# Kernel tuning notes

Measured on AMD Instinct MI355X. Metric: run time of the kernel, lower is better.

## Reference

```python
import jax, jax.numpy as jnp
import numpy as np

N = 50000
E = 800000
D = 256
C = 8
H = 64
LN_EPS = 1e-5


def setup_inputs() -> dict:
    key = jax.random.key(0)
    ks = jax.random.split(key, 8)
    x = jax.random.normal(ks[0], (N, D), dtype=jnp.float32)
    edge_index = jax.random.randint(ks[1], (2, E), 0, N, dtype=jnp.int64)
    omega = jax.random.uniform(ks[2], (E, C), dtype=jnp.float32)
    # xavier-uniform-ish parameter init
    def xavier(k, shape, fan_in, fan_out):
        a = float(np.sqrt(6.0 / (fan_in + fan_out)))
        return jax.random.uniform(k, shape, dtype=jnp.float32, minval=-a, maxval=a)
    proj = xavier(ks[3], (D, C, H), D, C * H)          # layer-0 projection
    W1 = xavier(ks[4], (C, H, H), H, H)                # layer-0 channel weights
    W2 = xavier(ks[5], (C, H, H), H, H)                # layer-1 channel weights
    ln_gamma = jnp.ones((H,), dtype=jnp.float32)
    ln_beta = jnp.zeros((H,), dtype=jnp.float32)
    return {"x": x, "edge_index": edge_index, "omega": omega,
            "proj": proj, "W1": W1, "W2": W2,
            "ln_gamma": ln_gamma, "ln_beta": ln_beta}


def _conv(h, src, dst, omega, W):
    # h: [N, C, H]; per-channel weighted scatter-add then channel-specific bmm.
    outs = []
    for c in range(C):  # small fixed channel loop, mirrors original structure
        msg = omega[:, c, None] * h[src, c, :]                  # [E, H]
        outs.append(jax.ops.segment_sum(msg, dst, num_segments=N))
    h_next = jnp.stack(outs, axis=1)                            # [N, C, H]
    return jnp.einsum('nch,cho->nco', h_next, W)                # channel bmm


def _layernorm(h, gamma, beta):
    mu = jnp.mean(h, axis=-1, keepdims=True)
    var = jnp.mean(jnp.square(h - mu), axis=-1, keepdims=True)
    return (h - mu) * jax.lax.rsqrt(var + LN_EPS) * gamma + beta


def reference(x, edge_index, omega, proj, W1, W2, ln_gamma, ln_beta):
    src, dst = edge_index[0], edge_index[1]
    # layer 0: project raw features into channel space [N, C, H]
    h = (x @ proj.reshape(D, C * H)).reshape(N, C, H)
    h = _conv(h, src, dst, omega, W1)
    h = _layernorm(h, ln_gamma, ln_beta)
    h = jax.nn.relu(h)
    # layer 1 (last layer: no ReLU)
    h = _conv(h, src, dst, omega, W2)
    h = _layernorm(h, ln_gamma, ln_beta)
    return h
```

## Files before the change

kernel.cpp:

```cpp
#include <hip/hip_runtime.h>

#define NN 50000
#define NE 800000
#define DD 256
#define CC 8
#define HH 64
#define CHW 512
#define LN_EPS 1e-5f
#define SCAN_BLOCKS ((NN + 1023) / 1024)

typedef __attribute__((ext_vector_type(8))) __bf16 bf16x8;
typedef __attribute__((ext_vector_type(4))) float f32x4;

__device__ inline ushort f2bf(float f) {
  uint u = __float_as_uint(f);
  return (ushort)((u + 0x7fffu + ((u >> 16) & 1u)) >> 16);
}

__device__ inline float omw_decode(uint w, int hi) {
  ushort hu = hi ? (ushort)(w >> 16) : (ushort)(w & 0xffffu);
  union { ushort u; _Float16 f; } cv; cv.u = hu;
  return (float)cv.f;
}

__device__ inline void acc8(float* acc, uint4 hv, float wt) {
  acc[0] += wt * __uint_as_float(hv.x << 16);
  acc[1] += wt * __uint_as_float(hv.x & 0xffff0000u);
  acc[2] += wt * __uint_as_float(hv.y << 16);
  acc[3] += wt * __uint_as_float(hv.y & 0xffff0000u);
  acc[4] += wt * __uint_as_float(hv.z << 16);
  acc[5] += wt * __uint_as_float(hv.z & 0xffff0000u);
  acc[6] += wt * __uint_as_float(hv.w << 16);
  acc[7] += wt * __uint_as_float(hv.w & 0xffff0000u);
}

__global__ __launch_bounds__(256) void fold_w1_kernel(
    const float* __restrict__ proj, const float* __restrict__ W1,
    ushort* __restrict__ projW1T) {
  __shared__ float wl[64];
  const int n = blockIdx.x;
  const int c = n >> 6, i = n & 63;
  const int tid = threadIdx.x;
  if (tid < 64) wl[tid] = W1[c * 4096 + tid * 64 + i];
  __syncthreads();
  const float* pr = proj + (size_t)tid * 512 + c * 64;
  float acc = 0.f;
#pragma unroll
  for (int k = 0; k < 64; ++k) acc += pr[k] * wl[k];
  projW1T[(size_t)n * 256 + tid] = f2bf(acc);
}

__global__ __launch_bounds__(256) void w2t_kernel(const float* __restrict__ W2,
                                                  ushort* __restrict__ W2T) {
  int c = blockIdx.x;
  for (int idx = threadIdx.x; idx < 4096; idx += 256) {
    int nn = idx >> 6, k = idx & 63;
    W2T[(size_t)c * 4096 + idx] = f2bf(W2[(size_t)c * 4096 + k * 64 + nn]);
  }
}

__global__ __launch_bounds__(256) void gemm_proj_kernel(
    const float* __restrict__ x, const ushort* __restrict__ BT,
    ushort* __restrict__ gout) {
  __shared__ ushort As[128 * 40];
  __shared__ ushort Bs[128 * 40];
  const int tid = threadIdx.x;
  const int lane = tid & 63, wv = tid >> 6;
  const int wm = wv >> 1, wn = wv & 1;
  const int lr = lane & 15, kg = lane >> 4;
  const int row0 = blockIdx.x * 128;
  const int col0 = blockIdx.y * 128;

  f32x4 acc[4][4];
#pragma unroll
  for (int i = 0; i < 4; ++i)
#pragma unroll
    for (int j = 0; j < 4; ++j) acc[i][j] = (f32x4){0.f, 0.f, 0.f, 0.f};

  for (int kk = 0; kk < 8; ++kk) {
    __syncthreads();
#pragma unroll
    for (int i = 0; i < 4; ++i) {
      int idx = tid + i * 256;
      int row = idx >> 3, quad = idx & 7;
      int rg = row0 + row;
      rg = rg < NN ? rg : NN - 1;
      float4 v = *(const float4*)(x + (size_t)rg * 256 + kk * 32 + quad * 4);
      ushort4 o = {f2bf(v.x), f2bf(v.y), f2bf(v.z), f2bf(v.w)};
      *(ushort4*)(As + row * 40 + quad * 4) = o;
    }
#pragma unroll
    for (int i = 0; i < 2; ++i) {
      int idx = tid + i * 256;
      int n = idx >> 2, quad = idx & 3;
      uint4 v = *(const uint4*)(BT + (size_t)(col0 + n) * 256 + kk * 32 + quad * 8);
      *(uint4*)(Bs + n * 40 + quad * 8) = v;
    }
    __syncthreads();
    bf16x8 a[4], b[4];
#pragma unroll
    for (int i = 0; i < 4; ++i)
      a[i] = *(const bf16x8*)(As + (wm * 64 + i * 16 + lr) * 40 + kg * 8);
#pragma unroll
    for (int j = 0; j < 4; ++j)
      b[j] = *(const bf16x8*)(Bs + (wn * 64 + j * 16 + lr) * 40 + kg * 8);
#pragma unroll
    for (int i = 0; i < 4; ++i)
#pragma unroll
      for (int j = 0; j < 4; ++j)
        acc[i][j] = __builtin_amdgcn_mfma_f32_16x16x32_bf16(a[i], b[j], acc[i][j], 0, 0, 0);
  }

  const int orow = kg * 4;
  const int ocol = lane & 15;
#pragma unroll
  for (int i = 0; i < 4; ++i) {
    int rg0 = row0 + wm * 64 + i * 16 + orow;
#pragma unroll
    for (int q = 0; q < 4; ++q) {
      int rg = rg0 + q;
      if (rg < NN) {
#pragma unroll
        for (int j = 0; j < 4; ++j) {
          gout[(size_t)rg * 512 + col0 + wn * 64 + j * 16 + ocol] = f2bf(acc[i][j][q]);
        }
      }
    }
  }
}

__global__ __launch_bounds__(256) void bmm_g_kernel(
    const ushort* __restrict__ h, const ushort* __restrict__ WT,
    ushort* __restrict__ g) {
  __shared__ ushort As[128 * 72];
  __shared__ ushort Bs[64 * 72];
  __shared__ float Cs[4][32 * 68];
  const int tid = threadIdx.x, lane = tid & 63, wv = tid >> 6;
  const int lr = lane & 15, kg = lane >> 4;
  const int n0 = blockIdx.x * 128;
  const int c = blockIdx.y;

#pragma unroll
  for (int i = 0; i < 4; ++i) {
    int idx = tid + i * 256;
    int row = idx >> 3, q = idx & 7;
    int rg = n0 + row;
    rg = rg < NN ? rg : NN - 1;
    *(uint4*)(As + row * 72 + q * 8) =
        *(const uint4*)(h + (size_t)rg * 512 + c * 64 + q * 8);
  }
#pragma unroll
  for (int i = 0; i < 2; ++i) {
    int idx = tid + i * 256;
    int row = idx >> 3, q = idx & 7;
    *(uint4*)(Bs + row * 72 + q * 8) =
        *(const uint4*)(WT + (size_t)c * 4096 + row * 64 + q * 8);
  }
  __syncthreads();

  f32x4 acc[2][4];
#pragma unroll
  for (int m = 0; m < 2; ++m)
#pragma unroll
    for (int j = 0; j < 4; ++j) acc[m][j] = (f32x4){0.f, 0.f, 0.f, 0.f};

#pragma unroll
  for (int ks = 0; ks < 2; ++ks) {
    bf16x8 a[2], b[4];
#pragma unroll
    for (int m = 0; m < 2; ++m)
      a[m] = *(const bf16x8*)(As + (wv * 32 + m * 16 + lr) * 72 + ks * 32 + kg * 8);
#pragma unroll
    for (int j = 0; j < 4; ++j)
      b[j] = *(const bf16x8*)(Bs + (j * 16 + lr) * 72 + ks * 32 + kg * 8);
#pragma unroll
    for (int m = 0; m < 2; ++m)
#pragma unroll
      for (int j = 0; j < 4; ++j)
        acc[m][j] = __builtin_amdgcn_mfma_f32_16x16x32_bf16(a[m], b[j], acc[m][j], 0, 0, 0);
  }

  float* cs = &Cs[wv][0];
#pragma unroll
  for (int m = 0; m < 2; ++m)
#pragma unroll
    for (int j = 0; j < 4; ++j)
#pragma unroll
      for (int q = 0; q < 4; ++q)
        cs[(m * 16 + kg * 4 + q) * 68 + j * 16 + lr] = acc[m][j][q];
  __syncthreads();

  const int row = lane & 31, half = lane >> 5;
  const int rg = n0 + wv * 32 + row;
  if (rg < NN) {
    const float* rp = cs + row * 68 + half * 32;
    ushort ob[32];
#pragma unroll
    for (int t = 0; t < 32; ++t) ob[t] = f2bf(rp[t]);
    ushort* op = g + (size_t)rg * 512 + c * 64 + half * 32;
#pragma unroll
    for (int t = 0; t < 4; ++t)
      *(uint4*)(op + t * 8) = *(uint4*)(ob + t * 8);
  }
}

__global__ void hist_kernel(const int* __restrict__ dst, int* __restrict__ cnt) {
  int e = blockIdx.x * 256 + threadIdx.x;
  if (e < NE) atomicAdd(&cnt[dst[e]], 1);
}

__global__ __launch_bounds__(1024) void scan1_kernel(const int* __restrict__ cnt,
                                                     int* __restrict__ blocksum) {
  __shared__ int ws[16];
  int tid = threadIdx.x, t = blockIdx.x * 1024 + tid;
  int v = (t < NN) ? cnt[t] : 0;
#pragma unroll
  for (int off = 32; off; off >>= 1) v += __shfl_xor(v, off);
  if ((tid & 63) == 0) ws[tid >> 6] = v;
  __syncthreads();
  if (tid < 16) {
    int s = ws[tid];
#pragma unroll
    for (int off = 8; off; off >>= 1) s += __shfl_xor(s, off, 16);
    if (tid == 0) blocksum[blockIdx.x] = s;
  }
}

__global__ __launch_bounds__(64) void scan2_kernel(int* __restrict__ blocksum,
                                                   int* __restrict__ rowptr) {
  int tid = threadIdx.x;
  int v = (tid < SCAN_BLOCKS) ? blocksum[tid] : 0;
  int orig = v;
#pragma unroll
  for (int off = 1; off < 64; off <<= 1) {
    int u = __shfl_up(v, off);
    if (tid >= off) v += u;
  }
  if (tid < SCAN_BLOCKS) blocksum[tid] = v - orig;
  if (tid == 63) rowptr[NN] = v;
}

__global__ __launch_bounds__(1024) void scan3_kernel(const int* __restrict__ blocksum,
                                                     int* __restrict__ cntcur,
                                                     int* __restrict__ rowptr) {
  __shared__ int ws[16];
  int tid = threadIdx.x, lane = tid & 63, wv = tid >> 6;
  int t = blockIdx.x * 1024 + tid;
  int orig = (t < NN) ? cntcur[t] : 0;
  int v = orig;
#pragma unroll
  for (int off = 1; off < 64; off <<= 1) {
    int u = __shfl_up(v, off);
    if (lane >= off) v += u;
  }
  if (lane == 63) ws[wv] = v;
  __syncthreads();
  if (tid < 16) {
    int s = ws[tid];
#pragma unroll
    for (int off = 1; off < 16; off <<= 1) {
      int u = __shfl_up(s, off, 16);
      if (tid >= off) s += u;
    }
    ws[tid] = s;
  }
  __syncthreads();
  if (t < NN) {
    int excl = blocksum[blockIdx.x] + (wv ? ws[wv - 1] : 0) + (v - orig);
    rowptr[t] = excl;
    cntcur[t] = excl;
  }
}

__global__ void fill_kernel(const int* __restrict__ dst, const int* __restrict__ src,
                            const float* __restrict__ omega, int* __restrict__ cursor,
                            int* __restrict__ esrc, uint4* __restrict__ eom) {
  int e = blockIdx.x * 256 + threadIdx.x;
  if (e < NE) {
    int d = dst[e];
    int pos = atomicAdd(&cursor[d], 1);
    esrc[pos] = src[e];
    const float4* om4 = (const float4*)(omega + (size_t)e * 8);
    float4 o0 = om4[0], o1 = om4[1];
    union { _Float16 f[8]; uint4 v; } pk;
    pk.f[0] = (_Float16)o0.x; pk.f[1] = (_Float16)o0.y;
    pk.f[2] = (_Float16)o0.z; pk.f[3] = (_Float16)o0.w;
    pk.f[4] = (_Float16)o1.x; pk.f[5] = (_Float16)o1.y;
    pk.f[6] = (_Float16)o1.z; pk.f[7] = (_Float16)o1.w;
    eom[pos] = pk.v;
  }
}

template <bool RELU, bool BF16OUT>
__global__ __launch_bounds__(256) void conv_ln_kernel(
    const ushort* __restrict__ g, const int* __restrict__ esrc,
    const uint* __restrict__ eomw, const int* __restrict__ rowptr,
    const float* __restrict__ gamma, const float* __restrict__ beta,
    void* __restrict__ outv) {
  int n = blockIdx.x * 4 + (threadIdx.x >> 6);
  if (n >= NN) return;
  const int lane = threadIdx.x & 63;
  const int c = lane >> 3;
  const int hi = c & 1;
  const int cw = c >> 1;
  const int i0 = (lane & 7) * 8;
  int start = rowptr[n], end = rowptr[n + 1];
  const uint4* g4 = (const uint4*)g;
  float acc[8] = {0.f, 0.f, 0.f, 0.f, 0.f, 0.f, 0.f, 0.f};

  int idx = start;
  for (; idx + 7 < end; idx += 8) {
    int s0 = esrc[idx + 0], s1 = esrc[idx + 1], s2 = esrc[idx + 2], s3 = esrc[idx + 3];
    int s4 = esrc[idx + 4], s5 = esrc[idx + 5], s6 = esrc[idx + 6], s7 = esrc[idx + 7];
    uint4 h0 = g4[(size_t)s0 * 64 + lane];
    uint4 h1 = g4[(size_t)s1 * 64 + lane];
    uint4 h2 = g4[(size_t)s2 * 64 + lane];
    uint4 h3 = g4[(size_t)s3 * 64 + lane];
    uint4 h4 = g4[(size_t)s4 * 64 + lane];
    uint4 h5 = g4[(size_t)s5 * 64 + lane];
    uint4 h6 = g4[(size_t)s6 * 64 + lane];
    uint4 h7 = g4[(size_t)s7 * 64 + lane];
    float w0 = omw_decode(eomw[(idx + 0) * 4 + cw], hi);
    float w1 = omw_decode(eomw[(idx + 1) * 4 + cw], hi);
    float w2 = omw_decode(eomw[(idx + 2) * 4 + cw], hi);
    float w3 = omw_decode(eomw[(idx + 3) * 4 + cw], hi);
    float w4 = omw_decode(eomw[(idx + 4) * 4 + cw], hi);
    float w5 = omw_decode(eomw[(idx + 5) * 4 + cw], hi);
    float w6 = omw_decode(eomw[(idx + 6) * 4 + cw], hi);
    float w7 = omw_decode(eomw[(idx + 7) * 4 + cw], hi);
    acc8(acc, h0, w0); acc8(acc, h1, w1); acc8(acc, h2, w2); acc8(acc, h3, w3);
    acc8(acc, h4, w4); acc8(acc, h5, w5); acc8(acc, h6, w6); acc8(acc, h7, w7);
  }
  for (; idx + 3 < end; idx += 4) {
    int s0 = esrc[idx + 0], s1 = esrc[idx + 1], s2 = esrc[idx + 2], s3 = esrc[idx + 3];
    uint4 h0 = g4[(size_t)s0 * 64 + lane];
    uint4 h1 = g4[(size_t)s1 * 64 + lane];
    uint4 h2 = g4[(size_t)s2 * 64 + lane];
    uint4 h3 = g4[(size_t)s3 * 64 + lane];
    float w0 = omw_decode(eomw[(idx + 0) * 4 + cw], hi);
    float w1 = omw_decode(eomw[(idx + 1) * 4 + cw], hi);
    float w2 = omw_decode(eomw[(idx + 2) * 4 + cw], hi);
    float w3 = omw_decode(eomw[(idx + 3) * 4 + cw], hi);
    acc8(acc, h0, w0); acc8(acc, h1, w1); acc8(acc, h2, w2); acc8(acc, h3, w3);
  }
  for (; idx < end; ++idx) {
    int s = esrc[idx];
    uint4 hv = g4[(size_t)s * 64 + lane];
    acc8(acc, hv, omw_decode(eomw[idx * 4 + cw], hi));
  }

  float s8 = ((acc[0] + acc[1]) + (acc[2] + acc[3])) +
             ((acc[4] + acc[5]) + (acc[6] + acc[7]));
  s8 += __shfl_xor(s8, 1);
  s8 += __shfl_xor(s8, 2);
  s8 += __shfl_xor(s8, 4);
  float mu = s8 * (1.f / 64.f);
  float d[8];
  float v = 0.f;
#pragma unroll
  for (int j = 0; j < 8; ++j) {
    d[j] = acc[j] - mu;
    v += d[j] * d[j];
  }
  v += __shfl_xor(v, 1);
  v += __shfl_xor(v, 2);
  v += __shfl_xor(v, 4);
  float inv = rsqrtf(v * (1.f / 64.f) + LN_EPS);
  float4 g0 = *(const float4*)(gamma + i0);
  float4 g1 = *(const float4*)(gamma + i0 + 4);
  float4 b0 = *(const float4*)(beta + i0);
  float4 b1 = *(const float4*)(beta + i0 + 4);
  float gg[8] = {g0.x, g0.y, g0.z, g0.w, g1.x, g1.y, g1.z, g1.w};
  float bb[8] = {b0.x, b0.y, b0.z, b0.w, b1.x, b1.y, b1.z, b1.w};
  float y[8];
#pragma unroll
  for (int j = 0; j < 8; ++j) {
    float t = d[j] * inv * gg[j] + bb[j];
    y[j] = RELU ? fmaxf(t, 0.f) : t;
  }
  if (BF16OUT) {
    ushort o[8];
#pragma unroll
    for (int j = 0; j < 8; ++j) o[j] = f2bf(y[j]);
    *(uint4*)((ushort*)outv + (size_t)n * 512 + c * 64 + i0) = *(uint4*)o;
  } else {
    float* op = (float*)outv + (size_t)n * 512 + c * 64 + i0;
    *(float4*)op = make_float4(y[0], y[1], y[2], y[3]);
    *(float4*)(op + 4) = make_float4(y[4], y[5], y[6], y[7]);
  }
}

extern "C" void kernel_launch(void* const* d_in, const int* in_sizes, int n_in,
                              void* d_out, int out_size, void* d_ws, size_t ws_size,
                              hipStream_t stream) {
  const float* x     = (const float*)d_in[0];
  const int*   edge  = (const int*)d_in[1];
  const float* omega = (const float*)d_in[2];
  const float* proj  = (const float*)d_in[3];
  const float* W1    = (const float*)d_in[4];
  const float* W2    = (const float*)d_in[5];
  const float* gamma = (const float*)d_in[6];
  const float* beta  = (const float*)d_in[7];
  const int* src = edge;
  const int* dst = edge + NE;

  char* p = (char*)d_ws;
  ushort* hbf    = (ushort*)p;              p += (size_t)NN * CHW * 2;
  uint4*  eom    = (uint4*)p;               p += (size_t)NE * 16;
  int*    esrc   = (int*)p;                 p += (size_t)NE * 4;
  int*    rowptr = (int*)p;                 p += (size_t)(NN + 16) * 4;
  int*    cntcur = (int*)p;                 p += (size_t)(NN + 16) * 4;
  int*    blocksum=(int*)p;                 p += (size_t)64 * 4;
  ushort* projW1T= (ushort*)p;              p += (size_t)512 * 256 * 2;
  ushort* W2T    = (ushort*)p;

  ushort* h1 = (ushort*)d_out;

  hipMemsetAsync(cntcur, 0, NN * sizeof(int), stream);
  hist_kernel<<<(NE + 255) / 256, 256, 0, stream>>>(dst, cntcur);
  scan1_kernel<<<SCAN_BLOCKS, 1024, 0, stream>>>(cntcur, blocksum);
  scan2_kernel<<<1, 64, 0, stream>>>(blocksum, rowptr);
  scan3_kernel<<<SCAN_BLOCKS, 1024, 0, stream>>>(blocksum, cntcur, rowptr);
  fill_kernel<<<(NE + 255) / 256, 256, 0, stream>>>(dst, src, omega, cntcur, esrc, eom);

  fold_w1_kernel<<<512, 256, 0, stream>>>(proj, W1, projW1T);
  w2t_kernel<<<8, 256, 0, stream>>>(W2, W2T);

  gemm_proj_kernel<<<dim3((NN + 127) / 128, 4), 256, 0, stream>>>(x, projW1T, hbf);
  conv_ln_kernel<true, true><<<(NN + 3) / 4, 256, 0, stream>>>(
      hbf, esrc, (const uint*)eom, rowptr, gamma, beta, h1);

  bmm_g_kernel<<<dim3((NN + 127) / 128, CC), 256, 0, stream>>>(h1, W2T, hbf);
  conv_ln_kernel<false, false><<<(NN + 3) / 4, 256, 0, stream>>>(
      hbf, esrc, (const uint*)eom, rowptr, gamma, beta, d_out);
}
```

Measured before the change: 414.3 us.

## Switch intermediates to channel-major layout and split conv per channel

Intermediate bf16 features are stored channel-major ([C][N][64]) instead of node-major, and the conv+layernorm kernel now launches one block per (4-node group, channel) with each lane handling one feature element. Consecutive blocks that share a channel gather from a 6.4 MB slice instead of the full 51 MB tensor, aiming for better L2 locality on the random gathers. In exchange, each edge's src index and omega weight are now read eight times across blocks, each lane loads 2 bytes instead of 16, and the block count grows eightfold.

After: 605.0 us. +46.0%, slower.

```diff
diff --git a/kernel.cpp b/kernel.cpp
--- a/kernel.cpp
+++ b/kernel.cpp
@@ -17,21 +17,14 @@
   return (ushort)((u + 0x7fffu + ((u >> 16) & 1u)) >> 16);
 }
 
+__device__ inline float b2f(ushort v) {
+  return __uint_as_float(((uint)v) << 16);
+}
+
 __device__ inline float omw_decode(uint w, int hi) {
   ushort hu = hi ? (ushort)(w >> 16) : (ushort)(w & 0xffffu);
   union { ushort u; _Float16 f; } cv; cv.u = hu;
   return (float)cv.f;
-}
-
-__device__ inline void acc8(float* acc, uint4 hv, float wt) {
-  acc[0] += wt * __uint_as_float(hv.x << 16);
-  acc[1] += wt * __uint_as_float(hv.x & 0xffff0000u);
-  acc[2] += wt * __uint_as_float(hv.y << 16);
-  acc[3] += wt * __uint_as_float(hv.y & 0xffff0000u);
-  acc[4] += wt * __uint_as_float(hv.z << 16);
-  acc[5] += wt * __uint_as_float(hv.z & 0xffff0000u);
-  acc[6] += wt * __uint_as_float(hv.w << 16);
-  acc[7] += wt * __uint_as_float(hv.w & 0xffff0000u);
 }
 
 __global__ __launch_bounds__(256) void fold_w1_kernel(
@@ -122,7 +115,9 @@
       if (rg < NN) {
 #pragma unroll
         for (int j = 0; j < 4; ++j) {
-          gout[(size_t)rg * 512 + col0 + wn * 64 + j * 16 + ocol] = f2bf(acc[i][j][q]);
+          int cc = col0 + wn * 64 + j * 16 + ocol;
+          int ch = cc >> 6, ii = cc & 63;
+          gout[((size_t)ch * NN + rg) * 64 + ii] = f2bf(acc[i][j][q]);
         }
       }
     }
@@ -139,6 +134,8 @@
   const int lr = lane & 15, kg = lane >> 4;
   const int n0 = blockIdx.x * 128;
   const int c = blockIdx.y;
+  const ushort* hc = h + (size_t)c * NN * 64;
+  ushort* gc = g + (size_t)c * NN * 64;
 
 #pragma unroll
   for (int i = 0; i < 4; ++i) {
@@ -146,8 +143,7 @@
     int row = idx >> 3, q = idx & 7;
     int rg = n0 + row;
     rg = rg < NN ? rg : NN - 1;
-    *(uint4*)(As + row * 72 + q * 8) =
-        *(const uint4*)(h + (size_t)rg * 512 + c * 64 + q * 8);
+    *(uint4*)(As + row * 72 + q * 8) = *(const uint4*)(hc + (size_t)rg * 64 + q * 8);
   }
 #pragma unroll
   for (int i = 0; i < 2; ++i) {
@@ -197,7 +193,7 @@
     ushort ob[32];
 #pragma unroll
     for (int t = 0; t < 32; ++t) ob[t] = f2bf(rp[t]);
-    ushort* op = g + (size_t)rg * 512 + c * 64 + half * 32;
+    ushort* op = gc + (size_t)rg * 64 + half * 32;
 #pragma unroll
     for (int t = 0; t < 4; ++t)
       *(uint4*)(op + t * 8) = *(uint4*)(ob + t * 8);
@@ -297,29 +293,29 @@
     const uint* __restrict__ eomw, const int* __restrict__ rowptr,
     const float* __restrict__ gamma, const float* __restrict__ beta,
     void* __restrict__ outv) {
-  int n = blockIdx.x * 4 + (threadIdx.x >> 6);
+  const int bid = blockIdx.x;
+  const int c = bid & 7;
+  const int n = (bid >> 3) * 4 + (threadIdx.x >> 6);
   if (n >= NN) return;
   const int lane = threadIdx.x & 63;
-  const int c = lane >> 3;
   const int hi = c & 1;
   const int cw = c >> 1;
-  const int i0 = (lane & 7) * 8;
   int start = rowptr[n], end = rowptr[n + 1];
-  const uint4* g4 = (const uint4*)g;
-  float acc[8] = {0.f, 0.f, 0.f, 0.f, 0.f, 0.f, 0.f, 0.f};
+  const ushort* gc = g + (size_t)c * NN * 64;
+  float acc = 0.f;
 
   int idx = start;
   for (; idx + 7 < end; idx += 8) {
     int s0 = esrc[idx + 0], s1 = esrc[idx + 1], s2 = esrc[idx + 2], s3 = esrc[idx + 3];
     int s4 = esrc[idx + 4], s5 = esrc[idx + 5], s6 = esrc[idx + 6], s7 = esrc[idx + 7];
-    uint4 h0 = g4[(size_t)s0 * 64 + lane];
-    uint4 h1 = g4[(size_t)s1 * 64 + lane];
-    uint4 h2 = g4[(size_t)s2 * 64 + lane];
-    uint4 h3 = g4[(size_t)s3 * 64 + lane];
-    uint4 h4 = g4[(size_t)s4 * 64 + lane];
-    uint4 h5 = g4[(size_t)s5 * 64 + lane];
-    uint4 h6 = g4[(size_t)s6 * 64 + lane];
-    uint4 h7 = g4[(size_t)s7 * 64 + lane];
+    ushort v0 = gc[(size_t)s0 * 64 + lane];
+    ushort v1 = gc[(size_t)s1 * 64 + lane];
+    ushort v2 = gc[(size_t)s2 * 64 + lane];
+    ushort v3 = gc[(size_t)s3 * 64 + lane];
+    ushort v4 = gc[(size_t)s4 * 64 + lane];
+    ushort v5 = gc[(size_t)s5 * 64 + lane];
+    ushort v6 = gc[(size_t)s6 * 64 + lane];
+    ushort v7 = gc[(size_t)s7 * 64 + lane];
     float w0 = omw_decode(eomw[(idx + 0) * 4 + cw], hi);
     float w1 = omw_decode(eomw[(idx + 1) * 4 + cw], hi);
     float w2 = omw_decode(eomw[(idx + 2) * 4 + cw], hi);
@@ -328,65 +324,44 @@
     float w5 = omw_decode(eomw[(idx + 5) * 4 + cw], hi);
     float w6 = omw_decode(eomw[(idx + 6) * 4 + cw], hi);
     float w7 = omw_decode(eomw[(idx + 7) * 4 + cw], hi);
-    acc8(acc, h0, w0); acc8(acc, h1, w1); acc8(acc, h2, w2); acc8(acc, h3, w3);
-    acc8(acc, h4, w4); acc8(acc, h5, w5); acc8(acc, h6, w6); acc8(acc, h7, w7);
+    acc += w0 * b2f(v0); acc += w1 * b2f(v1);
+    acc += w2 * b2f(v2); acc += w3 * b2f(v3);
+    acc += w4 * b2f(v4); acc += w5 * b2f(v5);
+    acc += w6 * b2f(v6); acc += w7 * b2f(v7);
   }
   for (; idx + 3 < end; idx += 4) {
     int s0 = esrc[idx + 0], s1 = esrc[idx + 1], s2 = esrc[idx + 2], s3 = esrc[idx + 3];
-    uint4 h0 = g4[(size_t)s0 * 64 + lane];
-    uint4 h1 = g4[(size_t)s1 * 64 + lane];
-    uint4 h2 = g4[(size_t)s2 * 64 + lane];
-    uint4 h3 = g4[(size_t)s3 * 64 + lane];
+    ushort v0 = gc[(size_t)s0 * 64 + lane];
+    ushort v1 = gc[(size_t)s1 * 64 + lane];
+    ushort v2 = gc[(size_t)s2 * 64 + lane];
+    ushort v3 = gc[(size_t)s3 * 64 + lane];
     float w0 = omw_decode(eomw[(idx + 0) * 4 + cw], hi);
     float w1 = omw_decode(eomw[(idx + 1) * 4 + cw], hi);
     float w2 = omw_decode(eomw[(idx + 2) * 4 + cw], hi);
     float w3 = omw_decode(eomw[(idx + 3) * 4 + cw], hi);
-    acc8(acc, h0, w0); acc8(acc, h1, w1); acc8(acc, h2, w2); acc8(acc, h3, w3);
+    acc += w0 * b2f(v0); acc += w1 * b2f(v1);
+    acc += w2 * b2f(v2); acc += w3 * b2f(v3);
   }
   for (; idx < end; ++idx) {
-    int s = esrc[idx];
-    uint4 hv = g4[(size_t)s * 64 + lane];
-    acc8(acc, hv, omw_decode(eomw[idx * 4 + cw], hi));
-  }
-
-  float s8 = ((acc[0] + acc[1]) + (acc[2] + acc[3])) +
-             ((acc[4] + acc[5]) + (acc[6] + acc[7]));
-  s8 += __shfl_xor(s8, 1);
-  s8 += __shfl_xor(s8, 2);
-  s8 += __shfl_xor(s8, 4);
-  float mu = s8 * (1.f / 64.f);
-  float d[8];
-  float v = 0.f;
-#pragma unroll
-  for (int j = 0; j < 8; ++j) {
-    d[j] = acc[j] - mu;
-    v += d[j] * d[j];
-  }
-  v += __shfl_xor(v, 1);
-  v += __shfl_xor(v, 2);
-  v += __shfl_xor(v, 4);
-  float inv = rsqrtf(v * (1.f / 64.f) + LN_EPS);
-  float4 g0 = *(const float4*)(gamma + i0);
-  float4 g1 = *(const float4*)(gamma + i0 + 4);
-  float4 b0 = *(const float4*)(beta + i0);
-  float4 b1 = *(const float4*)(beta + i0 + 4);
-  float gg[8] = {g0.x, g0.y, g0.z, g0.w, g1.x, g1.y, g1.z, g1.w};
-  float bb[8] = {b0.x, b0.y, b0.z, b0.w, b1.x, b1.y, b1.z, b1.w};
-  float y[8];
-#pragma unroll
-  for (int j = 0; j < 8; ++j) {
-    float t = d[j] * inv * gg[j] + bb[j];
-    y[j] = RELU ? fmaxf(t, 0.f) : t;
-  }
+    ushort v = gc[(size_t)esrc[idx] * 64 + lane];
+    acc += omw_decode(eomw[idx * 4 + cw], hi) * b2f(v);
+  }
+
+  float s = acc;
+#pragma unroll
+  for (int off = 32; off; off >>= 1) s += __shfl_xor(s, off);
+  float mu = s * (1.f / 64.f);
+  float d = acc - mu;
+  float v2 = d * d;
+#pragma unroll
+  for (int off = 32; off; off >>= 1) v2 += __shfl_xor(v2, off);
+  float inv = rsqrtf(v2 * (1.f / 64.f) + LN_EPS);
+  float y = d * inv * gamma[lane] + beta[lane];
+  if (RELU) y = fmaxf(y, 0.f);
   if (BF16OUT) {
-    ushort o[8];
-#pragma unroll
-    for (int j = 0; j < 8; ++j) o[j] = f2bf(y[j]);
-    *(uint4*)((ushort*)outv + (size_t)n * 512 + c * 64 + i0) = *(uint4*)o;
+    ((ushort*)outv)[((size_t)c * NN + n) * 64 + lane] = f2bf(y);
   } else {
-    float* op = (float*)outv + (size_t)n * 512 + c * 64 + i0;
-    *(float4*)op = make_float4(y[0], y[1], y[2], y[3]);
-    *(float4*)(op + 4) = make_float4(y[4], y[5], y[6], y[7]);
+    ((float*)outv)[(size_t)n * 512 + c * 64 + lane] = y;
   }
 }
 
@@ -426,11 +401,13 @@
   fold_w1_kernel<<<512, 256, 0, stream>>>(proj, W1, projW1T);
   w2t_kernel<<<8, 256, 0, stream>>>(W2, W2T);
 
+  const int conv_blocks = ((NN + 3) / 4) * 8;
+
   gemm_proj_kernel<<<dim3((NN + 127) / 128, 4), 256, 0, stream>>>(x, projW1T, hbf);
-  conv_ln_kernel<true, true><<<(NN + 3) / 4, 256, 0, stream>>>(
+  conv_ln_kernel<true, true><<<conv_blocks, 256, 0, stream>>>(
       hbf, esrc, (const uint*)eom, rowptr, gamma, beta, h1);
 
   bmm_g_kernel<<<dim3((NN + 127) / 128, CC), 256, 0, stream>>>(h1, W2T, hbf);
-  conv_ln_kernel<false, false><<<(NN + 3) / 4, 256, 0, stream>>>(
+  conv_ln_kernel<false, false><<<conv_blocks, 256, 0, stream>>>(
       hbf, esrc, (const uint*)eom, rowptr, gamma, beta, d_out);
 }
```
